# Kernel optimization log

Hardware: AMD Instinct MI355X
Metric: run time of the kernel (lower is better)

The kernel has to match this reference:

```python
import jax, jax.numpy as jnp
import numpy as np


def setup_inputs() -> dict:
    key = jax.random.key(0)
    k1, k2 = jax.random.split(key)
    x = jax.random.normal(k1, (16, 256, 128, 128), dtype=jnp.float32)
    # Conv2d(2, 1, 7, padding=3, bias=False) weight, OIHW layout
    conv_w = jax.random.normal(k2, (1, 2, 7, 7), dtype=jnp.float32) * 0.1
    return {"x": x, "conv_w": conv_w}


def reference(x, conv_w):
    # channel-wise mean and max pooling -> [B, 1, H, W] each
    avg_pool = jnp.mean(x, axis=1, keepdims=True)
    max_pool = jnp.max(x, axis=1, keepdims=True)
    cat = jnp.concatenate([avg_pool, max_pool], axis=1)  # [B, 2, H, W]
    # 7x7 conv, SAME padding (pad=3), NCHW / OIHW
    out = jax.lax.conv_general_dilated(
        cat, conv_w,
        window_strides=(1, 1),
        padding=((3, 3), (3, 3)),
        dimension_numbers=("NCHW", "OIHW", "NCHW"),
    )  # [B, 1, H, W]
    M = jax.nn.sigmoid(out)
    return x * M
```

## Files before the change

kernel.cpp:

```cpp
#include <hip/hip_runtime.h>
#include <math.h>

#define BB 16
#define CC 256
#define HH 128
#define WW 128
#define HWSZ (HH * WW)

typedef float floatx4 __attribute__((ext_vector_type(4)));

__global__ __launch_bounds__(256) void pool_kernel(const float* __restrict__ x,
                                                   float* __restrict__ avg_out,
                                                   float* __restrict__ max_out) {
    const int tf4   = threadIdx.x & 31;
    const int split = threadIdx.x >> 5;
    const int g0    = blockIdx.x * 32;
    const int p0    = g0 * 4;
    const int b     = p0 / HWSZ;
    const int hwb   = p0 % HWSZ;
    const int hw    = hwb + tf4 * 4;

    const float* xb = x + (size_t)b * CC * HWSZ + hw;

    float4 s = make_float4(0.f, 0.f, 0.f, 0.f);
    float4 m = make_float4(-INFINITY, -INFINITY, -INFINITY, -INFINITY);

    const int c0 = split * 32;
    #pragma unroll 8
    for (int i = 0; i < 32; ++i) {
        float4 v = *(const float4*)(xb + (size_t)(c0 + i) * HWSZ);
        s.x += v.x; s.y += v.y; s.z += v.z; s.w += v.w;
        m.x = fmaxf(m.x, v.x); m.y = fmaxf(m.y, v.y);
        m.z = fmaxf(m.z, v.z); m.w = fmaxf(m.w, v.w);
    }

    __shared__ float4 sS[8][32];
    __shared__ float4 sM[8][32];
    sS[split][tf4] = s;
    sM[split][tf4] = m;
    __syncthreads();

    for (int off = 4; off >= 1; off >>= 1) {
        if (split < off) {
            float4 a  = sS[split][tf4], bb2 = sS[split + off][tf4];
            a.x += bb2.x; a.y += bb2.y; a.z += bb2.z; a.w += bb2.w;
            sS[split][tf4] = a;
            float4 ma = sM[split][tf4], mb = sM[split + off][tf4];
            ma.x = fmaxf(ma.x, mb.x); ma.y = fmaxf(ma.y, mb.y);
            ma.z = fmaxf(ma.z, mb.z); ma.w = fmaxf(ma.w, mb.w);
            sM[split][tf4] = ma;
        }
        __syncthreads();
    }

    if (split == 0) {
        float4 a = sS[0][tf4];
        const float inv = 1.0f / CC;
        a.x *= inv; a.y *= inv; a.z *= inv; a.w *= inv;
        *(float4*)(avg_out + (size_t)b * HWSZ + hw) = a;
        *(float4*)(max_out + (size_t)b * HWSZ + hw) = sM[0][tf4];
    }
}

__global__ __launch_bounds__(256) void conv_kernel(const float* __restrict__ avg_in,
                                                   const float* __restrict__ max_in,
                                                   const float* __restrict__ wgt,
                                                   float* __restrict__ Mout) {
    __shared__ float sw[98];
    if (threadIdx.x < 98) sw[threadIdx.x] = wgt[threadIdx.x];
    __syncthreads();

    const int idx = blockIdx.x * blockDim.x + threadIdx.x;
    const int b  = idx / HWSZ;
    const int hw = idx % HWSZ;
    const int h  = hw >> 7;
    const int w  = hw & 127;

    const float* ap = avg_in + (size_t)b * HWSZ;
    const float* mp = max_in + (size_t)b * HWSZ;

    float acc = 0.f;
    #pragma unroll
    for (int kh = 0; kh < 7; ++kh) {
        const int hh = h + kh - 3;
        if (hh < 0 || hh >= HH) continue;
        #pragma unroll
        for (int kw = 0; kw < 7; ++kw) {
            const int ww2 = w + kw - 3;
            if (ww2 < 0 || ww2 >= WW) continue;
            const int off = hh * WW + ww2;
            acc += ap[off] * sw[kh * 7 + kw];
            acc += mp[off] * sw[49 + kh * 7 + kw];
        }
    }
    Mout[idx] = 1.0f / (1.0f + expf(-acc));
}

__global__ __launch_bounds__(256) void mul_kernel(const float* __restrict__ x,
                                                  const float* __restrict__ Mv,
                                                  float* __restrict__ out) {
    const int n4     = BB * CC * HWSZ / 4;
    const int stride = gridDim.x * blockDim.x;
    const int rbid   = gridDim.x - 1 - blockIdx.x;
    const int base   = rbid * blockDim.x + threadIdx.x;
    const int nIter  = n4 / stride;

    const floatx4* xv4 = (const floatx4*)x;
    floatx4*       ov4 = (floatx4*)out;

    for (int it = nIter - 1; it >= 0; --it) {
        const int i   = it * stride + base;
        const int b   = i >> 20;
        const int hw4 = i & 4095;
        floatx4 xv = __builtin_nontemporal_load(xv4 + i);
        floatx4 mv = *(const floatx4*)(Mv + (size_t)b * HWSZ + (size_t)hw4 * 4);
        floatx4 o  = xv * mv;
        __builtin_nontemporal_store(o, ov4 + i);
    }
}

extern "C" void kernel_launch(void* const* d_in, const int* in_sizes, int n_in,
                              void* d_out, int out_size, void* d_ws, size_t ws_size,
                              hipStream_t stream) {
    const float* x   = (const float*)d_in[0];
    const float* wgt = (const float*)d_in[1];
    float* out = (float*)d_out;

    float* avg_p = (float*)d_ws;
    float* max_p = avg_p + (size_t)BB * HWSZ;
    float* Mbuf  = max_p + (size_t)BB * HWSZ;

    pool_kernel<<<2048, 256, 0, stream>>>(x, avg_p, max_p);

    conv_kernel<<<(BB * HWSZ) / 256, 256, 0, stream>>>(avg_p, max_p, wgt, Mbuf);

    mul_kernel<<<4096, 256, 0, stream>>>(x, Mbuf, out);
}
```

Before: 145.6 us.

## Fuse pool, conv and multiply into one cooperative kernel with grid syncs

Merges the three separate launches (channel pooling, 7x7 conv + sigmoid, broadcast multiply) into a single persistent cooperative kernel. Grid-wide barriers separate the phases, and the grid size is taken from occupancy queries. This removes launch gaps between kernels but adds the cost of grid syncs and persistent-loop scheduling. The multiply phase also loses the reverse block ordering that the previous version used to reuse cached data.

```diff
diff --git a/kernel.cpp b/kernel.cpp
--- a/kernel.cpp
+++ b/kernel.cpp
@@ -1,5 +1,8 @@
 #include <hip/hip_runtime.h>
+#include <hip/hip_cooperative_groups.h>
 #include <math.h>
+
+namespace cg = cooperative_groups;
 
 #define BB 16
 #define CC 256
@@ -9,113 +12,116 @@
 
 typedef float floatx4 __attribute__((ext_vector_type(4)));
 
-__global__ __launch_bounds__(256) void pool_kernel(const float* __restrict__ x,
-                                                   float* __restrict__ avg_out,
-                                                   float* __restrict__ max_out) {
-    const int tf4   = threadIdx.x & 31;
-    const int split = threadIdx.x >> 5;
-    const int g0    = blockIdx.x * 32;
-    const int p0    = g0 * 4;
-    const int b     = p0 / HWSZ;
-    const int hwb   = p0 % HWSZ;
-    const int hw    = hwb + tf4 * 4;
-
-    const float* xb = x + (size_t)b * CC * HWSZ + hw;
-
-    float4 s = make_float4(0.f, 0.f, 0.f, 0.f);
-    float4 m = make_float4(-INFINITY, -INFINITY, -INFINITY, -INFINITY);
-
-    const int c0 = split * 32;
-    #pragma unroll 8
-    for (int i = 0; i < 32; ++i) {
-        float4 v = *(const float4*)(xb + (size_t)(c0 + i) * HWSZ);
-        s.x += v.x; s.y += v.y; s.z += v.z; s.w += v.w;
-        m.x = fmaxf(m.x, v.x); m.y = fmaxf(m.y, v.y);
-        m.z = fmaxf(m.z, v.z); m.w = fmaxf(m.w, v.w);
-    }
+__global__ __launch_bounds__(256) void fused_kernel(
+    const float* __restrict__ x, const float* __restrict__ wgt,
+    float* __restrict__ out, float* __restrict__ avg_p,
+    float* __restrict__ max_p, float* __restrict__ Mbuf)
+{
+    cg::grid_group grid = cg::this_grid();
+    const int nblk = gridDim.x;
+    const int nthr = nblk << 8;
 
     __shared__ float4 sS[8][32];
     __shared__ float4 sM[8][32];
-    sS[split][tf4] = s;
-    sM[split][tf4] = m;
-    __syncthreads();
+    __shared__ float  sw[98];
 
-    for (int off = 4; off >= 1; off >>= 1) {
-        if (split < off) {
-            float4 a  = sS[split][tf4], bb2 = sS[split + off][tf4];
-            a.x += bb2.x; a.y += bb2.y; a.z += bb2.z; a.w += bb2.w;
-            sS[split][tf4] = a;
-            float4 ma = sM[split][tf4], mb = sM[split + off][tf4];
-            ma.x = fmaxf(ma.x, mb.x); ma.y = fmaxf(ma.y, mb.y);
-            ma.z = fmaxf(ma.z, mb.z); ma.w = fmaxf(ma.w, mb.w);
-            sM[split][tf4] = ma;
-        }
-        __syncthreads();
-    }
-
-    if (split == 0) {
-        float4 a = sS[0][tf4];
-        const float inv = 1.0f / CC;
-        a.x *= inv; a.y *= inv; a.z *= inv; a.w *= inv;
-        *(float4*)(avg_out + (size_t)b * HWSZ + hw) = a;
-        *(float4*)(max_out + (size_t)b * HWSZ + hw) = sM[0][tf4];
-    }
-}
-
-__global__ __launch_bounds__(256) void conv_kernel(const float* __restrict__ avg_in,
-                                                   const float* __restrict__ max_in,
-                                                   const float* __restrict__ wgt,
-                                                   float* __restrict__ Mout) {
-    __shared__ float sw[98];
     if (threadIdx.x < 98) sw[threadIdx.x] = wgt[threadIdx.x];
     __syncthreads();
 
-    const int idx = blockIdx.x * blockDim.x + threadIdx.x;
-    const int b  = idx / HWSZ;
-    const int hw = idx % HWSZ;
-    const int h  = hw >> 7;
-    const int w  = hw & 127;
+    {
+        const int tf4   = threadIdx.x & 31;
+        const int split = threadIdx.x >> 5;
+        const int c0    = split * 32;
 
-    const float* ap = avg_in + (size_t)b * HWSZ;
-    const float* mp = max_in + (size_t)b * HWSZ;
+        for (int tile = blockIdx.x; tile < 2048; tile += nblk) {
+            const int p0 = tile * 128;
+            const int b  = p0 >> 14;
+            const int hw = (p0 & (HWSZ - 1)) + tf4 * 4;
+            const float* xb = x + (size_t)b * CC * HWSZ + hw;
 
-    float acc = 0.f;
-    #pragma unroll
-    for (int kh = 0; kh < 7; ++kh) {
-        const int hh = h + kh - 3;
-        if (hh < 0 || hh >= HH) continue;
-        #pragma unroll
-        for (int kw = 0; kw < 7; ++kw) {
-            const int ww2 = w + kw - 3;
-            if (ww2 < 0 || ww2 >= WW) continue;
-            const int off = hh * WW + ww2;
-            acc += ap[off] * sw[kh * 7 + kw];
-            acc += mp[off] * sw[49 + kh * 7 + kw];
+            float4 s = make_float4(0.f, 0.f, 0.f, 0.f);
+            float4 m = make_float4(-INFINITY, -INFINITY, -INFINITY, -INFINITY);
+            #pragma unroll 8
+            for (int i = 0; i < 32; ++i) {
+                float4 v = *(const float4*)(xb + (size_t)(c0 + i) * HWSZ);
+                s.x += v.x; s.y += v.y; s.z += v.z; s.w += v.w;
+                m.x = fmaxf(m.x, v.x); m.y = fmaxf(m.y, v.y);
+                m.z = fmaxf(m.z, v.z); m.w = fmaxf(m.w, v.w);
+            }
+            sS[split][tf4] = s;
+            sM[split][tf4] = m;
+            __syncthreads();
+
+            for (int off = 4; off >= 1; off >>= 1) {
+                if (split < off) {
+                    float4 a  = sS[split][tf4], b2 = sS[split + off][tf4];
+                    a.x += b2.x; a.y += b2.y; a.z += b2.z; a.w += b2.w;
+                    sS[split][tf4] = a;
+                    float4 ma = sM[split][tf4], mb = sM[split + off][tf4];
+                    ma.x = fmaxf(ma.x, mb.x); ma.y = fmaxf(ma.y, mb.y);
+                    ma.z = fmaxf(ma.z, mb.z); ma.w = fmaxf(ma.w, mb.w);
+                    sM[split][tf4] = ma;
+                }
+                __syncthreads();
+            }
+
+            if (split == 0) {
+                float4 a = sS[0][tf4];
+                const float inv = 1.0f / CC;
+                a.x *= inv; a.y *= inv; a.z *= inv; a.w *= inv;
+                *(float4*)(avg_p + (size_t)b * HWSZ + hw) = a;
+                *(float4*)(max_p + (size_t)b * HWSZ + hw) = sM[0][tf4];
+            }
+            __syncthreads();
         }
     }
-    Mout[idx] = 1.0f / (1.0f + expf(-acc));
-}
 
-__global__ __launch_bounds__(256) void mul_kernel(const float* __restrict__ x,
-                                                  const float* __restrict__ Mv,
-                                                  float* __restrict__ out) {
-    const int n4     = BB * CC * HWSZ / 4;
-    const int stride = gridDim.x * blockDim.x;
-    const int rbid   = gridDim.x - 1 - blockIdx.x;
-    const int base   = rbid * blockDim.x + threadIdx.x;
-    const int nIter  = n4 / stride;
+    __threadfence();
+    grid.sync();
 
-    const floatx4* xv4 = (const floatx4*)x;
-    floatx4*       ov4 = (floatx4*)out;
+    {
+        for (int idx = (blockIdx.x << 8) + threadIdx.x; idx < BB * HWSZ; idx += nthr) {
+            const int b  = idx >> 14;
+            const int hw = idx & (HWSZ - 1);
+            const int h  = hw >> 7;
+            const int w  = hw & 127;
 
-    for (int it = nIter - 1; it >= 0; --it) {
-        const int i   = it * stride + base;
-        const int b   = i >> 20;
-        const int hw4 = i & 4095;
-        floatx4 xv = __builtin_nontemporal_load(xv4 + i);
-        floatx4 mv = *(const floatx4*)(Mv + (size_t)b * HWSZ + (size_t)hw4 * 4);
-        floatx4 o  = xv * mv;
-        __builtin_nontemporal_store(o, ov4 + i);
+            const float* ap = avg_p + (size_t)b * HWSZ;
+            const float* mp = max_p + (size_t)b * HWSZ;
+
+            float acc = 0.f;
+            #pragma unroll
+            for (int kh = 0; kh < 7; ++kh) {
+                const int hh = h + kh - 3;
+                if (hh < 0 || hh >= HH) continue;
+                #pragma unroll
+                for (int kw = 0; kw < 7; ++kw) {
+                    const int ww2 = w + kw - 3;
+                    if (ww2 < 0 || ww2 >= WW) continue;
+                    const int off = hh * WW + ww2;
+                    acc += ap[off] * sw[kh * 7 + kw];
+                    acc += mp[off] * sw[49 + kh * 7 + kw];
+                }
+            }
+            Mbuf[idx] = 1.0f / (1.0f + expf(-acc));
+        }
+    }
+
+    __threadfence();
+    grid.sync();
+
+    {
+        const int n4 = BB * CC * HWSZ / 4;
+        const floatx4* xv4 = (const floatx4*)x;
+        floatx4*       ov4 = (floatx4*)out;
+
+        for (int i = (blockIdx.x << 8) + threadIdx.x; i < n4; i += nthr) {
+            const int b   = i >> 20;
+            const int hw4 = i & 4095;
+            floatx4 xv = __builtin_nontemporal_load(xv4 + i);
+            floatx4 mv = *(const floatx4*)(Mbuf + ((size_t)b << 14) + (hw4 << 2));
+            __builtin_nontemporal_store(xv * mv, ov4 + i);
+        }
     }
 }
 
@@ -130,9 +136,14 @@
     float* max_p = avg_p + (size_t)BB * HWSZ;
     float* Mbuf  = max_p + (size_t)BB * HWSZ;
 
-    pool_kernel<<<2048, 256, 0, stream>>>(x, avg_p, max_p);
+    int maxPerCU = 0;
+    hipOccupancyMaxActiveBlocksPerMultiprocessor(&maxPerCU, (const void*)fused_kernel, 256, 0);
+    if (maxPerCU < 1) maxPerCU = 1;
+    int grid = maxPerCU * 256;
+    if (grid > 2048) grid = 2048;
 
-    conv_kernel<<<(BB * HWSZ) / 256, 256, 0, stream>>>(avg_p, max_p, wgt, Mbuf);
-
-    mul_kernel<<<4096, 256, 0, stream>>>(x, Mbuf, out);
+    void* args[] = {(void*)&x, (void*)&wgt, (void*)&out,
+                    (void*)&avg_p, (void*)&max_p, (void*)&Mbuf};
+    hipLaunchCooperativeKernel((void*)fused_kernel, dim3(grid), dim3(256),
+                               args, 0, stream);
 }
```

Result: slower. 389.5 us (+167.5%).
